# Kernel optimization log

Hardware: AMD Instinct MI355X
Metric: run time of the kernel (lower is better)

The kernel has to match this reference:

```python
import jax, jax.numpy as jnp
import numpy as np

N = 2048        # tokens (batch*seq)
H = 4096        # hidden_size (LLaMA-7B)
I = 11008       # intermediate_size (LLaMA-7B)
QMAX = 127.0    # int8 symmetric quant range


def setup_inputs() -> dict:
    key = jax.random.key(0)
    ks = jax.random.split(key, 6)
    # pre-quantized int8 activations (stored as int32) + per-token dynamic scales
    x_q = jax.random.randint(ks[0], (N, H), -127, 128, dtype=jnp.int32)
    x_scale = jax.random.uniform(ks[1], (N,), dtype=jnp.float32) * 0.01 + 1e-4
    # fused [gate; up] int8 weight [2I, H] with per-output-channel scales
    w_gateup = jax.random.randint(ks[2], (2 * I, H), -127, 128, dtype=jnp.int32)
    w_gateup_scale = jax.random.uniform(ks[3], (2 * I,), dtype=jnp.float32) * 0.005 + 1e-4
    # down_proj int8 weight [H, I] with per-output-channel scales
    w_down = jax.random.randint(ks[4], (H, I), -127, 128, dtype=jnp.int32)
    w_down_scale = jax.random.uniform(ks[5], (H,), dtype=jnp.float32) * 0.005 + 1e-4
    return {"x_q": x_q, "x_scale": x_scale, "w_gateup": w_gateup,
            "w_gateup_scale": w_gateup_scale, "w_down": w_down,
            "w_down_scale": w_down_scale}


def reference(x_q, x_scale, w_gateup, w_gateup_scale, w_down, w_down_scale):
    acc = jnp.matmul(x_q, w_gateup.T)                      # [N, 2I] int32
    gateup = acc.astype(jnp.float32) * x_scale[:, None] * w_gateup_scale[None, :]
    # --- fused silu_and_mul + dynamic per-token requantization ---
    gate, up = jnp.split(gateup, 2, axis=-1)               # each [N, I]
    act = jax.nn.silu(gate) * up                           # [N, I]
    s2 = jnp.max(jnp.abs(act), axis=-1) / QMAX             # [N] dynamic scale
    q2 = jnp.clip(jnp.round(act / s2[:, None]), -QMAX, QMAX)  # requantized int8 (as f32)
    out = jnp.matmul(q2, w_down.T.astype(jnp.float32)) * s2[:, None] * w_down_scale[None, :]
    return out                                             # [N, H]
```

## Files before the change

kernel.cpp:

```cpp
#include <hip/hip_runtime.h>
#include <stdint.h>

typedef int i32x4 __attribute__((ext_vector_type(4)));
typedef unsigned short u16x8 __attribute__((ext_vector_type(8)));

#define N_TOK 2048
#define HID   4096
#define INTER 11008
#define TWOI  22016
#define KT1   64
#define KT2   172

#define GLD16(gp, lp) __builtin_amdgcn_global_load_lds( \
    (const __attribute__((address_space(1))) void*)(gp), \
    (__attribute__((address_space(3))) void*)(lp), 16, 0, 0)
#define BAR() __builtin_amdgcn_s_barrier()
#define WVM(n) asm volatile("s_waitcnt vmcnt(" #n ")" ::: "memory")
#define LGKM0() do { asm volatile("s_waitcnt lgkmcnt(0)" ::: "memory"); \
                     __builtin_amdgcn_sched_barrier(0); } while (0)

__device__ __forceinline__ unsigned short f2bf(float f) {
  uint32_t u = __float_as_uint(f);
  uint32_t r = (u + 0x7fffu + ((u >> 16) & 1u)) >> 16;
  return (unsigned short)r;
}

__device__ __forceinline__ float bf2f(unsigned short b) {
  return __uint_as_float(((uint32_t)b) << 16);
}

__global__ __launch_bounds__(256) void pack_frag(
    const int* __restrict__ src, uint8_t* __restrict__ dst,
    int lgPR, int KT, int K)
{
  const int u = blockIdx.x * 256 + threadIdx.x;
  const int l = u & 63;
  const int rest = u >> 6;
  const int f = rest & ((1 << (lgPR - 4)) - 1);
  const int s = rest >> (lgPR - 4);
  const int p = s / KT;
  const int kt = s - p * KT;
  const int row = (p << lgPR) + f * 16 + (l & 15);
  const int col = kt * 64 + ((l >> 4) << 4);
  const int* sp = src + (size_t)row * K + col;
  i32x4 o;
#pragma unroll
  for (int qq = 0; qq < 4; ++qq) {
    i32x4 w = *reinterpret_cast<const i32x4*>(sp + qq * 4);
    o[qq] = (w[0] & 255) | ((w[1] & 255) << 8) | ((w[2] & 255) << 16)
          | ((w[3] & 255) << 24);
  }
  *reinterpret_cast<i32x4*>(dst + (size_t)u * 16) = o;
}

__global__ __launch_bounds__(512, 2) void gemm1_k(
    const uint8_t* __restrict__ x8p, const uint8_t* __restrict__ wgp,
    const float* __restrict__ xs, const float* __restrict__ wgs,
    unsigned short* __restrict__ gu)
{
  __shared__ uint8_t sm[131072];
  const int tid = threadIdx.x;
  const int lane = tid & 63, wid = tid >> 6;
  const int wgm = wid >> 2, wgn = wid & 3;
  const int r15 = lane & 15;
  const int l16 = lane * 16;
  const int aBase = (wgm << 13) + l16;
  const int bBase = 16384 + (wgn << 12) + l16;

  const int bid = blockIdx.x;
  const int v = (bid & 7) * 86 + (bid >> 3);
  const int mt = v & 7;
  const int ntB = v >> 3;

  const uint8_t* pA = x8p + (size_t)mt  * (KT1 * 16384) + tid * 16;
  const uint8_t* pB = wgp + (size_t)ntB * (KT1 * 16384) + tid * 16;

  i32x4 acc[8][4] = {};

#define STG1(t, s) do {                                        \
    uint8_t* l = sm + (s) * 32768 + tid * 16;                  \
    const uint8_t* aa = pA + (size_t)(t) * 16384;              \
    GLD16(aa, l);                                              \
    GLD16(aa + 8192, l + 8192);                                \
    const uint8_t* bb = pB + (size_t)(t) * 16384;              \
    GLD16(bb, l + 16384);                                      \
    GLD16(bb + 8192, l + 24576);                               \
  } while (0)

  STG1(0, 0); STG1(1, 1); STG1(2, 2);
  WVM(8); BAR();

  for (int t = 0; t < KT1; ++t) {
    const int rem = KT1 - 1 - t;
    const uint8_t* b = sm + (t & 3) * 32768;
    uint8_t* lnx = sm + ((t + 3) & 3) * 32768 + tid * 16;
    i32x4 bv[4], av[4];
#pragma unroll
    for (int n = 0; n < 4; ++n)
      bv[n] = *reinterpret_cast<const i32x4*>(b + bBase + n * 1024);
#pragma unroll
    for (int m = 0; m < 4; ++m)
      av[m] = *reinterpret_cast<const i32x4*>(b + aBase + m * 1024);
    if (rem >= 3) {
      const uint8_t* bb = pB + (size_t)(t + 3) * 16384;
      GLD16(bb, lnx + 16384);
      GLD16(bb + 8192, lnx + 24576);
    }
    BAR();
    LGKM0();
    __builtin_amdgcn_s_setprio(1);
#pragma unroll
    for (int m = 0; m < 4; ++m)
#pragma unroll
      for (int n = 0; n < 4; ++n)
        acc[m][n] = __builtin_amdgcn_mfma_i32_16x16x64_i8(
            av[m], bv[n], acc[m][n], 0, 0, 0);
    __builtin_amdgcn_s_setprio(0);
#pragma unroll
    for (int m = 0; m < 4; ++m)
      av[m] = *reinterpret_cast<const i32x4*>(b + aBase + (m + 4) * 1024);
    if (rem >= 3) {
      const uint8_t* aa = pA + (size_t)(t + 3) * 16384;
      GLD16(aa, lnx);
      GLD16(aa + 8192, lnx + 8192);
      WVM(8);
    } else if (rem == 2) { WVM(4); }
    else if (rem == 1)   { WVM(0); }
    BAR();
    LGKM0();
    __builtin_amdgcn_s_setprio(1);
#pragma unroll
    for (int m = 0; m < 4; ++m)
#pragma unroll
      for (int n = 0; n < 4; ++n)
        acc[m + 4][n] = __builtin_amdgcn_mfma_i32_16x16x64_i8(
            av[m], bv[n], acc[m + 4][n], 0, 0, 0);
    __builtin_amdgcn_s_setprio(0);
  }
#undef STG1

  const int rq = (lane >> 4) << 2;
#pragma unroll
  for (int m = 0; m < 8; ++m) {
#pragma unroll
    for (int r = 0; r < 4; ++r) {
      const int rowl = (wgm << 7) + m * 16 + rq + r;
      const int grow = mt * 256 + rowl;
      const float xr = xs[grow];
      const int colb = ntB * 256 + (wgn << 6) + r15;
      unsigned short* op = gu + (size_t)grow * TWOI + colb;
      const float* wp = wgs + colb;
#pragma unroll
      for (int n = 0; n < 4; ++n)
        op[n * 16] = f2bf((float)acc[m][n][r] * xr * wp[n * 16]);
    }
  }
}

__global__ __launch_bounds__(256) void rowmax_k(
    const unsigned short* __restrict__ gu, float* __restrict__ mx)
{
  const int row = blockIdx.x;
  const unsigned short* gp = gu + (size_t)row * TWOI;
  float m = 0.f;
  for (int i = threadIdx.x; i < INTER / 8; i += 256) {
    u16x8 gv = *reinterpret_cast<const u16x8*>(gp + i * 8);
    u16x8 uv = *reinterpret_cast<const u16x8*>(gp + INTER + i * 8);
#pragma unroll
    for (int j = 0; j < 8; ++j) {
      float gf = bf2f(gv[j]);
      float uf = bf2f(uv[j]);
      float a = (gf / (1.f + __expf(-gf))) * uf;
      m = fmaxf(m, __builtin_fabsf(a));
    }
  }
#pragma unroll
  for (int o = 32; o; o >>= 1) m = fmaxf(m, __shfl_xor(m, o, 64));
  __shared__ float red[4];
  const int lane = threadIdx.x & 63, wid = threadIdx.x >> 6;
  if (lane == 0) red[wid] = m;
  __syncthreads();
  if (threadIdx.x == 0)
    mx[row] = fmaxf(fmaxf(red[0], red[1]), fmaxf(red[2], red[3]));
}

__global__ __launch_bounds__(256) void quant_k(
    const unsigned short* __restrict__ gu, const float* __restrict__ mx,
    uint8_t* __restrict__ q2p)
{
  const int u = blockIdx.x * 256 + threadIdx.x;
  const int l = u & 63;
  const int rest = u >> 6;
  const int f = rest & 7;
  const int s = rest >> 3;
  const int mt = s / KT2;
  const int t = s - mt * KT2;
  const int row = mt * 128 + f * 16 + (l & 15);
  const int col = t * 64 + ((l >> 4) << 4);
  const unsigned short* gp = gu + (size_t)row * TWOI + col;
  const float inv = 127.0f / fmaxf(mx[row], 1e-30f);
  u16x8 g0 = *reinterpret_cast<const u16x8*>(gp);
  u16x8 g1 = *reinterpret_cast<const u16x8*>(gp + 8);
  u16x8 u0 = *reinterpret_cast<const u16x8*>(gp + INTER);
  u16x8 u1 = *reinterpret_cast<const u16x8*>(gp + INTER + 8);
  i32x4 o;
#pragma unroll
  for (int qq = 0; qq < 4; ++qq) {
    uint32_t d = 0;
#pragma unroll
    for (int b = 0; b < 4; ++b) {
      const int j = qq * 4 + b;
      float gf = bf2f((j < 8) ? g0[j] : g1[j - 8]);
      float uf = bf2f((j < 8) ? u0[j] : u1[j - 8]);
      float a = (gf / (1.f + __expf(-gf))) * uf;
      float rr = rintf(a * inv);
      rr = fminf(fmaxf(rr, -127.f), 127.f);
      d |= ((uint32_t)((int)rr & 255)) << (8 * b);
    }
    o[qq] = (int)d;
  }
  *reinterpret_cast<i32x4*>(q2p + (size_t)u * 16) = o;
}

__global__ __launch_bounds__(512, 2) void gemm2_k(
    const uint8_t* __restrict__ q2p, const uint8_t* __restrict__ wdp,
    const float* __restrict__ mx, const float* __restrict__ wds,
    float* __restrict__ out)
{
  __shared__ uint8_t sm[98304];
  const int tid = threadIdx.x;
  const int lane = tid & 63, wid = tid >> 6;
  const int wgm = wid >> 2, wgn = wid & 3;
  const int r15 = lane & 15;
  const int l16 = lane * 16;
  const int aBase = (wgm << 12) + l16;
  const int bBase = 8192 + (wgn << 12) + l16;

  const int bid = blockIdx.x;
  const int v = (bid & 7) * 32 + (bid >> 3);
  const int nt = v >> 4, mt = v & 15;

  const uint8_t* pA = q2p + (size_t)mt * (KT2 * 8192)  + tid * 16;
  const uint8_t* pB = wdp + (size_t)nt * (KT2 * 16384) + tid * 16;

  i32x4 acc[4][4] = {};

#define STG2(t, s) do {                                        \
    uint8_t* l = sm + (s) * 24576 + tid * 16;                  \
    GLD16(pA + (size_t)(t) * 8192, l);                         \
    const uint8_t* bb = pB + (size_t)(t) * 16384;              \
    GLD16(bb, l + 8192);                                       \
    GLD16(bb + 8192, l + 16384);                               \
  } while (0)

  STG2(0, 0); STG2(1, 1); STG2(2, 2);
  WVM(6); BAR();

  for (int t = 0; t < KT2; ++t) {
    const int rem = KT2 - 1 - t;
    const uint8_t* b = sm + (t & 3) * 24576;
    uint8_t* lnx = sm + ((t + 3) & 3) * 24576 + tid * 16;
    i32x4 bv[4], av[2];
#pragma unroll
    for (int n = 0; n < 4; ++n)
      bv[n] = *reinterpret_cast<const i32x4*>(b + bBase + n * 1024);
#pragma unroll
    for (int m = 0; m < 2; ++m)
      av[m] = *reinterpret_cast<const i32x4*>(b + aBase + m * 1024);
    if (rem >= 3) {
      const uint8_t* bb = pB + (size_t)(t + 3) * 16384;
      GLD16(bb, lnx + 8192);
      GLD16(bb + 8192, lnx + 16384);
    }
    BAR();
    LGKM0();
    __builtin_amdgcn_s_setprio(1);
#pragma unroll
    for (int m = 0; m < 2; ++m)
#pragma unroll
      for (int n = 0; n < 4; ++n)
        acc[m][n] = __builtin_amdgcn_mfma_i32_16x16x64_i8(
            av[m], bv[n], acc[m][n], 0, 0, 0);
    __builtin_amdgcn_s_setprio(0);
#pragma unroll
    for (int m = 0; m < 2; ++m)
      av[m] = *reinterpret_cast<const i32x4*>(b + aBase + (m + 2) * 1024);
    if (rem >= 3) {
      GLD16(pA + (size_t)(t + 3) * 8192, lnx);
      WVM(6);
    } else if (rem == 2) { WVM(3); }
    else if (rem == 1)   { WVM(0); }
    BAR();
    LGKM0();
    __builtin_amdgcn_s_setprio(1);
#pragma unroll
    for (int m = 0; m < 2; ++m)
#pragma unroll
      for (int n = 0; n < 4; ++n)
        acc[m + 2][n] = __builtin_amdgcn_mfma_i32_16x16x64_i8(
            av[m], bv[n], acc[m + 2][n], 0, 0, 0);
    __builtin_amdgcn_s_setprio(0);
  }
#undef STG2

  const int rq = (lane >> 4) << 2;
#pragma unroll
  for (int m = 0; m < 4; ++m) {
#pragma unroll
    for (int r = 0; r < 4; ++r) {
      const int rowl = (wgm << 6) + m * 16 + rq + r;
      const int grow = mt * 128 + rowl;
      const float s2 = mx[grow] * (1.0f / 127.0f);
      float* op = out + (size_t)grow * HID + nt * 256 + (wgn << 6) + r15;
      const float* wp = wds + nt * 256 + (wgn << 6) + r15;
#pragma unroll
      for (int n = 0; n < 4; ++n)
        op[n * 16] = (float)acc[m][n][r] * s2 * wp[n * 16];
    }
  }
}

extern "C" void kernel_launch(void* const* d_in, const int* in_sizes, int n_in,
                              void* d_out, int out_size, void* d_ws, size_t ws_size,
                              hipStream_t stream)
{
  const int*   x_q = (const int*)d_in[0];
  const float* xs  = (const float*)d_in[1];
  const int*   wg  = (const int*)d_in[2];
  const float* wgs = (const float*)d_in[3];
  const int*   wd  = (const int*)d_in[4];
  const float* wds = (const float*)d_in[5];
  float* out = (float*)d_out;

  uint8_t* ws = (uint8_t*)d_ws;
  uint8_t* x8p = ws;
  uint8_t* wgp = x8p + 8388608;
  uint8_t* wdp = wgp + 90177536;
  unsigned short* gu = (unsigned short*)(wdp + 45088768);
  float* mx = (float*)((uint8_t*)gu + 90177536);
  uint8_t* q2p = (uint8_t*)mx + 8192;

  pack_frag<<<2048, 256, 0, stream>>>(x_q, x8p, 8, KT1, HID);
  pack_frag<<<22016, 256, 0, stream>>>(wg, wgp, 8, KT1, HID);
  pack_frag<<<11008, 256, 0, stream>>>(wd, wdp, 8, KT2, INTER);

  gemm1_k<<<688, 512, 0, stream>>>(x8p, wgp, xs, wgs, gu);
  rowmax_k<<<N_TOK, 256, 0, stream>>>(gu, mx);
  quant_k<<<5504, 256, 0, stream>>>(gu, mx, q2p);
  gemm2_k<<<256, 512, 0, stream>>>(q2p, wdp, mx, wds, out);
}
```

Measured before the change: 436.3 us.

## Fuse SiLU-mul and row-max into gemm1 epilogue via interleaved gate/up packing

The gate/up weight is repacked so that each 16-column fragment pair holds matching gate and up channels. This lets gemm1's epilogue compute silu(gate)*up directly and write only the bf16 activation of width I, not the 2I-wide gateup buffer. Per-row absolute maxima are reduced with shuffles and combined across blocks using integer atomicMax on float bits into a zeroed buffer. This removes the rowmax kernel and halves the intermediate traffic that quant_k reads. The cost is atomics and extra transcendental work in the GEMM epilogue.

```diff
diff --git a/kernel.cpp b/kernel.cpp
--- a/kernel.cpp
+++ b/kernel.cpp
@@ -53,10 +53,39 @@
   *reinterpret_cast<i32x4*>(dst + (size_t)u * 16) = o;
 }
 
+__global__ __launch_bounds__(256) void pack_gufrag(
+    const int* __restrict__ src, uint8_t* __restrict__ dst)
+{
+  const int u = blockIdx.x * 256 + threadIdx.x;
+  const int l = u & 63;
+  const int rest = u >> 6;
+  const int fi = rest & 15;
+  const int s = rest >> 4;
+  const int p = s / KT1;
+  const int kt = s - p * KT1;
+  const int base = p * 128 + ((fi >> 1) << 4) + (l & 15);
+  const int srow = (fi & 1) ? (INTER + base) : base;
+  const int col = kt * 64 + ((l >> 4) << 4);
+  const int* sp = src + (size_t)srow * HID + col;
+  i32x4 o;
+#pragma unroll
+  for (int qq = 0; qq < 4; ++qq) {
+    i32x4 w = *reinterpret_cast<const i32x4*>(sp + qq * 4);
+    o[qq] = (w[0] & 255) | ((w[1] & 255) << 8) | ((w[2] & 255) << 16)
+          | ((w[3] & 255) << 24);
+  }
+  *reinterpret_cast<i32x4*>(dst + (size_t)u * 16) = o;
+}
+
+__global__ __launch_bounds__(1024) void zero_mx(float* __restrict__ mx) {
+  const int i = blockIdx.x * 1024 + threadIdx.x;
+  if (i < N_TOK) mx[i] = 0.0f;
+}
+
 __global__ __launch_bounds__(512, 2) void gemm1_k(
     const uint8_t* __restrict__ x8p, const uint8_t* __restrict__ wgp,
     const float* __restrict__ xs, const float* __restrict__ wgs,
-    unsigned short* __restrict__ gu)
+    unsigned short* __restrict__ act, float* __restrict__ mx)
 {
   __shared__ uint8_t sm[131072];
   const int tid = threadIdx.x;
@@ -142,50 +171,40 @@
   const int rq = (lane >> 4) << 2;
 #pragma unroll
   for (int m = 0; m < 8; ++m) {
-#pragma unroll
-    for (int r = 0; r < 4; ++r) {
-      const int rowl = (wgm << 7) + m * 16 + rq + r;
-      const int grow = mt * 256 + rowl;
-      const float xr = xs[grow];
-      const int colb = ntB * 256 + (wgn << 6) + r15;
-      unsigned short* op = gu + (size_t)grow * TWOI + colb;
-      const float* wp = wgs + colb;
-#pragma unroll
-      for (int n = 0; n < 4; ++n)
-        op[n * 16] = f2bf((float)acc[m][n][r] * xr * wp[n * 16]);
-    }
-  }
-}
-
-__global__ __launch_bounds__(256) void rowmax_k(
-    const unsigned short* __restrict__ gu, float* __restrict__ mx)
-{
-  const int row = blockIdx.x;
-  const unsigned short* gp = gu + (size_t)row * TWOI;
-  float m = 0.f;
-  for (int i = threadIdx.x; i < INTER / 8; i += 256) {
-    u16x8 gv = *reinterpret_cast<const u16x8*>(gp + i * 8);
-    u16x8 uv = *reinterpret_cast<const u16x8*>(gp + INTER + i * 8);
-#pragma unroll
-    for (int j = 0; j < 8; ++j) {
-      float gf = bf2f(gv[j]);
-      float uf = bf2f(uv[j]);
-      float a = (gf / (1.f + __expf(-gf))) * uf;
-      m = fmaxf(m, __builtin_fabsf(a));
-    }
-  }
-#pragma unroll
-  for (int o = 32; o; o >>= 1) m = fmaxf(m, __shfl_xor(m, o, 64));
-  __shared__ float red[4];
-  const int lane = threadIdx.x & 63, wid = threadIdx.x >> 6;
-  if (lane == 0) red[wid] = m;
-  __syncthreads();
-  if (threadIdx.x == 0)
-    mx[row] = fmaxf(fmaxf(red[0], red[1]), fmaxf(red[2], red[3]));
+    float am[4] = {0.f, 0.f, 0.f, 0.f};
+#pragma unroll
+    for (int p = 0; p < 2; ++p) {
+      const int colb = ntB * 128 + (wgn << 5) + (p << 4) + r15;
+      const float gsc = wgs[colb];
+      const float usc = wgs[INTER + colb];
+#pragma unroll
+      for (int r = 0; r < 4; ++r) {
+        const int rowl = (wgm << 7) + m * 16 + rq + r;
+        const int grow = mt * 256 + rowl;
+        const float xr = xs[grow];
+        const float g  = (float)acc[m][2 * p][r] * xr * gsc;
+        const float uv = (float)acc[m][2 * p + 1][r] * xr * usc;
+        const float a  = g / (1.f + __expf(-g)) * uv;
+        act[(size_t)grow * INTER + colb] = f2bf(a);
+        am[r] = fmaxf(am[r], __builtin_fabsf(a));
+      }
+    }
+#pragma unroll
+    for (int r = 0; r < 4; ++r)
+#pragma unroll
+      for (int off = 1; off < 16; off <<= 1)
+        am[r] = fmaxf(am[r], __shfl_xor(am[r], off, 64));
+    if (r15 == 0) {
+#pragma unroll
+      for (int r = 0; r < 4; ++r)
+        atomicMax((int*)&mx[mt * 256 + (wgm << 7) + m * 16 + rq + r],
+                  __float_as_int(am[r]));
+    }
+  }
 }
 
 __global__ __launch_bounds__(256) void quant_k(
-    const unsigned short* __restrict__ gu, const float* __restrict__ mx,
+    const unsigned short* __restrict__ act, const float* __restrict__ mx,
     uint8_t* __restrict__ q2p)
 {
   const int u = blockIdx.x * 256 + threadIdx.x;
@@ -197,12 +216,10 @@
   const int t = s - mt * KT2;
   const int row = mt * 128 + f * 16 + (l & 15);
   const int col = t * 64 + ((l >> 4) << 4);
-  const unsigned short* gp = gu + (size_t)row * TWOI + col;
+  const unsigned short* ap = act + (size_t)row * INTER + col;
   const float inv = 127.0f / fmaxf(mx[row], 1e-30f);
-  u16x8 g0 = *reinterpret_cast<const u16x8*>(gp);
-  u16x8 g1 = *reinterpret_cast<const u16x8*>(gp + 8);
-  u16x8 u0 = *reinterpret_cast<const u16x8*>(gp + INTER);
-  u16x8 u1 = *reinterpret_cast<const u16x8*>(gp + INTER + 8);
+  u16x8 a0 = *reinterpret_cast<const u16x8*>(ap);
+  u16x8 a1 = *reinterpret_cast<const u16x8*>(ap + 8);
   i32x4 o;
 #pragma unroll
   for (int qq = 0; qq < 4; ++qq) {
@@ -210,10 +227,8 @@
 #pragma unroll
     for (int b = 0; b < 4; ++b) {
       const int j = qq * 4 + b;
-      float gf = bf2f((j < 8) ? g0[j] : g1[j - 8]);
-      float uf = bf2f((j < 8) ? u0[j] : u1[j - 8]);
-      float a = (gf / (1.f + __expf(-gf))) * uf;
-      float rr = rintf(a * inv);
+      float af = bf2f((j < 8) ? a0[j] : a1[j - 8]);
+      float rr = rintf(af * inv);
       rr = fminf(fmaxf(rr, -127.f), 127.f);
       d |= ((uint32_t)((int)rr & 255)) << (8 * b);
     }
@@ -336,16 +351,16 @@
   uint8_t* x8p = ws;
   uint8_t* wgp = x8p + 8388608;
   uint8_t* wdp = wgp + 90177536;
-  unsigned short* gu = (unsigned short*)(wdp + 45088768);
-  float* mx = (float*)((uint8_t*)gu + 90177536);
+  unsigned short* act = (unsigned short*)(wdp + 45088768);
+  float* mx = (float*)((uint8_t*)act + 45088768);
   uint8_t* q2p = (uint8_t*)mx + 8192;
 
+  zero_mx<<<2, 1024, 0, stream>>>(mx);
   pack_frag<<<2048, 256, 0, stream>>>(x_q, x8p, 8, KT1, HID);
-  pack_frag<<<22016, 256, 0, stream>>>(wg, wgp, 8, KT1, HID);
+  pack_gufrag<<<22016, 256, 0, stream>>>(wg, wgp);
   pack_frag<<<11008, 256, 0, stream>>>(wd, wdp, 8, KT2, INTER);
 
-  gemm1_k<<<688, 512, 0, stream>>>(x8p, wgp, xs, wgs, gu);
-  rowmax_k<<<N_TOK, 256, 0, stream>>>(gu, mx);
-  quant_k<<<5504, 256, 0, stream>>>(gu, mx, q2p);
+  gemm1_k<<<688, 512, 0, stream>>>(x8p, wgp, xs, wgs, act, mx);
+  quant_k<<<5504, 256, 0, stream>>>(act, mx, q2p);
   gemm2_k<<<256, 512, 0, stream>>>(q2p, wdp, mx, wds, out);
 }
```

Result: no change. 433.4 us (-0.7%).
